# Kernel tuning notes

Hardware: AMD Instinct MI355X
Metric: run time of the kernel (lower is better)

The kernel has to match this reference:

```python
import jax, jax.numpy as jnp
import numpy as np

NUM_NODES = 50000
NUM_RELATIONS = 16
HIDDEN = 128
NUM_LAYERS = 3
NUM_EDGES = 1600000


def setup_inputs() -> dict:
    key = jax.random.key(0)
    ks = jax.random.split(key, 6)
    edge_index = jax.random.randint(ks[0], (2, NUM_EDGES), 0, NUM_NODES, dtype=jnp.int64)
    edge_type = jax.random.randint(ks[1], (NUM_EDGES,), 0, NUM_RELATIONS, dtype=jnp.int64)
    scale = 1.0 / np.sqrt(HIDDEN)
    node_init = jax.random.normal(ks[2], (NUM_NODES, HIDDEN), dtype=jnp.float32) * scale
    W = jax.random.normal(ks[3], (NUM_LAYERS, NUM_RELATIONS, HIDDEN, HIDDEN), dtype=jnp.float32) * scale
    root = jax.random.normal(ks[4], (NUM_LAYERS, HIDDEN, HIDDEN), dtype=jnp.float32) * scale
    bias = jnp.zeros((NUM_LAYERS, HIDDEN), dtype=jnp.float32)
    return {"edge_index": edge_index, "edge_type": edge_type,
            "node_init": node_init, "W": W, "root": root, "bias": bias}


def _fast_rgcn_layer(x, src, tgt, edge_type, W_r, root_r, bias_r):
    # FastRGCNConv with aggr='mean': mean of messages per (target node, relation),
    # message = x_src @ W[relation]. By linearity, aggregate normalized x_src per
    # (node, relation) first, then apply relation weights with a single einsum.
    N, d = x.shape
    R = W_r.shape[0]
    seg = tgt * R + edge_type                       # combined (node, relation) segment id
    msg = x[src]                                    # [E, d] irregular gather
    agg = jax.ops.segment_sum(msg, seg, num_segments=N * R).reshape(N, R, d)
    cnt = jax.ops.segment_sum(jnp.ones_like(edge_type, dtype=x.dtype), seg,
                              num_segments=N * R).reshape(N, R, 1)
    agg = agg / jnp.clip(cnt, 1.0, None)            # per-(node,relation) mean
    out = jnp.einsum('nrd,rdo->no', agg, W_r)       # relation-specific transform
    out = out + x @ root_r + bias_r                 # root/self connection + bias
    return out


def reference(edge_index, edge_type, node_init, W, root, bias):
    src, tgt = edge_index[0], edge_index[1]
    x = node_init
    for i in range(NUM_LAYERS):
        x = _fast_rgcn_layer(x, src, tgt, edge_type, W[i], root[i], bias[i])
        if i < NUM_LAYERS - 1:
            x = jax.nn.relu(x)  # dropout omitted (eval mode)
    return x
```

## Files before the change

### kernel.cpp

```cpp
#include <hip/hip_runtime.h>
#include <hip/hip_bf16.h>

#define N_NODES   50000
#define N_REL     16
#define HID       128
#define N_EDGES   1600000
#define N_TILES   3125
#define N_BINS    800000
#define N_RUNS    50000
#define N_SCANBLK 49
#define N_MBLK    1563
#define PAYLOAD_CAP 2400064
#define BS_LAYER  278528
#define AG_STRIDE 136

typedef unsigned short ushort_t;
typedef __attribute__((ext_vector_type(8))) short short8;
typedef __attribute__((ext_vector_type(4))) float f32x4;

union BF2U { __hip_bfloat162 h; unsigned u; };

__device__ __forceinline__ unsigned pack_bf16_2(float x, float y) {
  BF2U c; c.h = __float22bfloat162_rn(make_float2(x, y));
  return c.u;
}


__global__ __launch_bounds__(256) void k_zero(int* p, int n) {
  int i = blockIdx.x * 256 + threadIdx.x;
  if (i < n) p[i] = 0;
}

__global__ __launch_bounds__(256) void k_hist(const int* __restrict__ ei,
                                              const int* __restrict__ et,
                                              int* __restrict__ cnt) {
  int e = blockIdx.x * 256 + threadIdx.x;
  int tgt = ei[N_EDGES + e];
  int r   = et[e];
  int key = ((tgt >> 4) << 8) | (r << 4) | (tgt & 15);
  atomicAdd(&cnt[key], 1);
}

__global__ __launch_bounds__(256) void k_runpad(const int* __restrict__ cnt,
                                                int* __restrict__ padtot) {
  int r = blockIdx.x * 256 + threadIdx.x;
  if (r >= N_RUNS) return;
  const int4* c4 = (const int4*)(cnt + r * 16);
  int s = 0;
#pragma unroll
  for (int j = 0; j < 4; ++j) { int4 v = c4[j]; s += v.x + v.y + v.z + v.w; }
  padtot[r] = (s + 15) & ~15;
}

__global__ __launch_bounds__(256) void k_btot(const int* __restrict__ in,
                                              int* __restrict__ totals, int n) {
  __shared__ int s[256];
  int t = threadIdx.x, b = blockIdx.x;
  int sum = 0;
  for (int j = 0; j < 4; ++j) {
    int idx = b * 1024 + j * 256 + t;
    sum += (idx < n) ? in[idx] : 0;
  }
  s[t] = sum; __syncthreads();
  for (int ofs = 128; ofs > 0; ofs >>= 1) {
    if (t < ofs) s[t] += s[t + ofs];
    __syncthreads();
  }
  if (t == 0) totals[b] = s[0];
}

__global__ __launch_bounds__(1024) void k_scan_totals(int* totals, int* endp, int nblk) {
  __shared__ int s[1024];
  int t = threadIdx.x;
  int v = (t < nblk) ? totals[t] : 0;
  s[t] = v; __syncthreads();
  for (int ofs = 1; ofs < 1024; ofs <<= 1) {
    int x = (t >= ofs) ? s[t - ofs] : 0;
    __syncthreads();
    s[t] += x;
    __syncthreads();
  }
  if (t < nblk) totals[t] = s[t] - v;
  if (t == nblk - 1) *endp = s[t];
}

__global__ __launch_bounds__(1024) void k_scan_within(int* __restrict__ a,
                                                      const int* __restrict__ totals,
                                                      int n) {
  __shared__ int s[1024];
  int t = threadIdx.x, blk = blockIdx.x;
  int b = blk * 1024 + t;
  int v = (b < n) ? a[b] : 0;
  s[t] = v; __syncthreads();
  for (int ofs = 1; ofs < 1024; ofs <<= 1) {
    int x = (t >= ofs) ? s[t - ofs] : 0;
    __syncthreads();
    s[t] += x;
    __syncthreads();
  }
  if (b < n) a[b] = totals[blk] + s[t] - v;
}

__global__ __launch_bounds__(256) void k_fineoff(const int* __restrict__ cnt,
                                                 const int* __restrict__ run_start,
                                                 int* __restrict__ cursors,
                                                 unsigned* __restrict__ payload) {
  int r = blockIdx.x * 256 + threadIdx.x;
  if (r >= N_RUNS) return;
  int base = run_start[r];
  int e1   = run_start[r + 1];
  int pfx = 0;
  for (int i = 0; i < 16; ++i) {
    cursors[r * 16 + i] = base + pfx;
    pfx += cnt[r * 16 + i];
  }
  const unsigned dummy = ((unsigned)N_NODES << 16) | (1u << 4) | 15u;
  for (int j = base + pfx; j < e1; ++j) payload[j] = dummy;
}

__global__ __launch_bounds__(256) void k_sort(const int* __restrict__ ei,
                                              const int* __restrict__ et,
                                              const int* __restrict__ cnt,
                                              int* __restrict__ cursors,
                                              unsigned* __restrict__ payload) {
  int e = blockIdx.x * 256 + threadIdx.x;
  int src = ei[e];
  int tgt = ei[N_EDGES + e];
  int r   = et[e];
  int key = ((tgt >> 4) << 8) | (r << 4) | (tgt & 15);
  int c = cnt[key]; c = c > 4095 ? 4095 : c;
  int pos = atomicAdd(&cursors[key], 1);
  payload[pos] = ((unsigned)src << 16) | ((unsigned)c << 4) | (unsigned)(tgt & 15);
}

__global__ __launch_bounds__(256) void k_bt(const float* __restrict__ W,
                                            const float* __restrict__ root,
                                            ushort_t* __restrict__ Bs) {
  int idx = blockIdx.x * 256 + threadIdx.x;
  int l    = idx / BS_LAYER;
  int rem  = idx - l * BS_LAYER;
  int frag = rem >> 9;
  int wi   = rem & 511;
  int lane = wi >> 3;
  int j    = wi & 7;
  int cb   = frag & 7;
  int kk   = (frag >> 3) & 3;
  int r    = frag >> 5;
  int col  = cb * 16 + (lane & 15);
  int d    = kk * 32 + (lane >> 4) * 8 + j;
  float v;
  if (r < 16) v = W[((size_t)(l * N_REL + r) * HID + d) * HID + col];
  else        v = root[((size_t)l * HID + d) * HID + col];
  __hip_bfloat16 h = __float2bfloat16(v);
  union { __hip_bfloat16 h; ushort_t u; } c; c.h = h;
  Bs[idx] = c.u;
}

__global__ __launch_bounds__(256) void k_xh(const float* __restrict__ xin,
                                            ushort_t* __restrict__ xh) {
  int i = blockIdx.x * 256 + threadIdx.x;
  float4 v = ((const float4*)xin)[i];
  uint2 u;
  u.x = pack_bf16_2(v.x, v.y);
  u.y = pack_bf16_2(v.z, v.w);
  ((uint2*)xh)[i] = u;
}

__global__ __launch_bounds__(256) void k_zrow(ushort_t* xa, ushort_t* xb) {
  int t = threadIdx.x;
  if (t < 128) xa[(size_t)N_NODES * HID + t] = 0;
  else         xb[(size_t)N_NODES * HID + (t - 128)] = 0;
}


__global__ __launch_bounds__(256, 3) void k_main(const ushort_t* __restrict__ xh,
                                                 ushort_t* __restrict__ xh_out,
                                                 float* __restrict__ fout,
                                                 const ushort_t* __restrict__ Bs,
                                                 const float* __restrict__ bias,
                                                 const int* __restrict__ run_start,
                                                 const unsigned* __restrict__ payload,
                                                 int write_f32) {
  __shared__ alignas(16) ushort_t agg[2][2][32][AG_STRIDE];

  const int tile0 = blockIdx.x * 2;
  const int tid   = threadIdx.x;
  const int wave  = tid >> 6;
  const int lane  = tid & 63;
  const int m16   = lane & 15;
  const int q     = lane >> 4;
  const unsigned* xh32 = (const unsigned*)xh;

  if (wave < 2) {
    const int p = wave;
    int ebv = 0;
    {
      int s8 = lane >> 2, t2 = (lane >> 1) & 1, h = lane & 1;
      int tt = tile0 + t2;
      int idx = (tt < N_TILES) ? (tt * 16 + s8 * 2 + p + h) : N_RUNS;
      if (lane < 32) ebv = run_start[idx];
    }
    int pv[8][2];
#pragma unroll
    for (int s = 0; s < 8; ++s)
#pragma unroll
      for (int t = 0; t < 2; ++t) {
        int e0 = __builtin_amdgcn_readlane(ebv, s * 4 + t * 2);
        pv[s][t] = (int)payload[e0 + lane];
      }

#define ISSUE16(DST, PV, JB)                                                  \
    _Pragma("unroll")                                                         \
    for (int k1 = 0; k1 < 16; ++k1) {                                         \
      unsigned spq = (unsigned)__builtin_amdgcn_readlane(PV, (JB) + k1);      \
      DST[k1] = xh32[(spq >> 16) * 64 + lane];                                \
    }

#define FLUSHM(TB, BUF)                                                       \
    if (mcur >= 0) {                                                          \
      float sc = __builtin_amdgcn_rcpf((float)scnt);                          \
      *(unsigned*)&agg[BUF][p][(TB) + mcur][lane * 2] =                       \
          pack_bf16_2(a0 * sc, a1 * sc);                                      \
    }

#define CONSUME1(SPK, XV, TB, BUF)                                            \
    {                                                                         \
      int mk = (int)((SPK) & 15u);                                            \
      if (mk != mcur) {                                                       \
        FLUSHM(TB, BUF);                                                      \
        mcur = mk; scnt = (int)(((SPK) >> 4) & 4095u);                        \
        a0 = 0.f; a1 = 0.f;                                                   \
      }                                                                       \
      a0 += __uint_as_float((XV) << 16);                                      \
      a1 += __uint_as_float((XV) & 0xffff0000u);                              \
    }

#define CONS16(PV, JB, SLOT, TB, BUF)                                         \
    _Pragma("unroll")                                                         \
    for (int k2 = 0; k2 < 16; ++k2) {                                         \
      unsigned spk = (unsigned)__builtin_amdgcn_readlane(PV, (JB) + k2);      \
      CONSUME1(spk, SLOT[k2], TB, BUF);                                       \
    }

#define RUNC(E0, E1, PV, S0, S1a, S1b, TB, BUF)                               \
    {                                                                         \
      int cnt = (E1) - (E0);                                                  \
      int mcur = -1, scnt = 1;                                                \
      float a0 = 0.f, a1 = 0.f;                                               \
      if (cnt > 0) {                                                          \
        if (cnt > 16) { ISSUE16(S1a, PV, 16); }                               \
        CONS16(PV, 0, S0, TB, BUF);                                           \
        if (cnt > 16) {                                                       \
          if (cnt > 32) { ISSUE16(S1b, PV, 32); }                             \
          CONS16(PV, 16, S1a, TB, BUF);                                       \
          if (cnt > 32) {                                                     \
            if (cnt > 48) { ISSUE16(S1a, PV, 48); }                           \
            CONS16(PV, 32, S1b, TB, BUF);                                     \
            if (cnt > 48) { CONS16(PV, 48, S1a, TB, BUF); }                   \
          }                                                                   \
        }                                                                     \
        for (int c0 = (E0) + 64; c0 < (E1); c0 += 16) {             \
          int pvx = (int)payload[c0 + lane];                                  \
          unsigned xv[16];                                                    \
          ISSUE16(xv, pvx, 0);                                                \
          CONS16(pvx, 0, xv, TB, BUF);                                        \
        }                                                                     \
        FLUSHM(TB, BUF);                                                      \
      }                                                                       \
    }

    unsigned xqA[16], xqB[16], xqC[16], xqD[16];
    ISSUE16(xqA, pv[0][0], 0);
    ISSUE16(xqB, pv[0][1], 0);

#pragma unroll
    for (int s = 0; s < 8; ++s) {
      const int buf = s & 1;
      {
        short8 z = {0, 0, 0, 0, 0, 0, 0, 0};
#pragma unroll
        for (int i = 0; i < 8; ++i)
          *(short8*)&agg[buf][p][i * 4 + q][m16 * 8] = z;
      }
      int e00 = __builtin_amdgcn_readlane(ebv, s * 4 + 0);
      int e01 = __builtin_amdgcn_readlane(ebv, s * 4 + 1);
      int e10 = __builtin_amdgcn_readlane(ebv, s * 4 + 2);
      int e11 = __builtin_amdgcn_readlane(ebv, s * 4 + 3);
      RUNC(e00, e01, pv[s][0], xqA, xqC, xqD, 0, buf);
      RUNC(e10, e11, pv[s][1], xqB, xqC, xqD, 16, buf);
      if (s < 7) {
        ISSUE16(xqA, pv[s + 1][0], 0);
        ISSUE16(xqB, pv[s + 1][1], 0);
      }
      __syncthreads();
    }
#undef RUNC
#undef CONS16
#undef CONSUME1
#undef FLUSHM
#undef ISSUE16
    return;
  }

  const int c = wave - 2;
  f32x4 acc[2][4];
#pragma unroll
  for (int t = 0; t < 2; ++t)
#pragma unroll
    for (int i = 0; i < 4; ++i) acc[t][i] = (f32x4){0.f, 0.f, 0.f, 0.f};

  for (int s = 0; s < 8; ++s) {
    __syncthreads();
#pragma unroll
    for (int rp = 0; rp < 2; ++rp) {
      int rel = s * 2 + rp;
      short8 Bf[4][4];
#pragma unroll
      for (int kk = 0; kk < 4; ++kk)
#pragma unroll
        for (int i = 0; i < 4; ++i)
          Bf[kk][i] = *(const short8*)(Bs +
              ((size_t)((rel * 4 + kk) * 8 + (c * 4 + i)) << 9) + lane * 8);
#pragma unroll
      for (int kk = 0; kk < 4; ++kk) {
        short8 A0 = *(const short8*)&agg[s & 1][rp][m16][kk * 32 + q * 8];
        short8 A1 = *(const short8*)&agg[s & 1][rp][16 + m16][kk * 32 + q * 8];
#pragma unroll
        for (int i = 0; i < 4; ++i) {
          acc[0][i] = __builtin_amdgcn_mfma_f32_16x16x32_bf16(A0, Bf[kk][i], acc[0][i], 0, 0, 0);
          acc[1][i] = __builtin_amdgcn_mfma_f32_16x16x32_bf16(A1, Bf[kk][i], acc[1][i], 0, 0, 0);
        }
      }
    }
  }

  {
    short8 Bf[4][4];
#pragma unroll
    for (int kk = 0; kk < 4; ++kk)
#pragma unroll
      for (int i = 0; i < 4; ++i)
        Bf[kk][i] = *(const short8*)(Bs +
            ((size_t)((16 * 4 + kk) * 8 + (c * 4 + i)) << 9) + lane * 8);
    int r0 = tile0 * 16 + m16;      if (r0 > N_NODES) r0 = N_NODES;
    int r1 = tile0 * 16 + 16 + m16; if (r1 > N_NODES) r1 = N_NODES;
#pragma unroll
    for (int kk = 0; kk < 4; ++kk) {
      short8 A0 = *(const short8*)(xh + (size_t)r0 * HID + kk * 32 + q * 8);
      short8 A1 = *(const short8*)(xh + (size_t)r1 * HID + kk * 32 + q * 8);
#pragma unroll
      for (int i = 0; i < 4; ++i) {
        acc[0][i] = __builtin_amdgcn_mfma_f32_16x16x32_bf16(A0, Bf[kk][i], acc[0][i], 0, 0, 0);
        acc[1][i] = __builtin_amdgcn_mfma_f32_16x16x32_bf16(A1, Bf[kk][i], acc[1][i], 0, 0, 0);
      }
    }
  }

  float bvv[4];
#pragma unroll
  for (int i = 0; i < 4; ++i) bvv[i] = bias[(c * 4 + i) * 16 + m16];
  int rbase = tile0 * 16 + q * 4;
#pragma unroll
  for (int t = 0; t < 2; ++t)
#pragma unroll
    for (int rg = 0; rg < 4; ++rg) {
      int row = rbase + t * 16 + rg;
      if (row < N_NODES) {
#pragma unroll
        for (int i = 0; i < 4; ++i) {
          float v = acc[t][i][rg] + bvv[i];
          int col = (c * 4 + i) * 16 + m16;
          if (write_f32) {
            fout[(size_t)row * HID + col] = v;
          } else {
            v = fmaxf(v, 0.f);
            union { __hip_bfloat16 h; ushort_t u; } cv;
            cv.h = __float2bfloat16(v);
            xh_out[(size_t)row * HID + col] = cv.u;
          }
        }
      }
    }
}


extern "C" void kernel_launch(void* const* d_in, const int* in_sizes, int n_in,
                              void* d_out, int out_size, void* d_ws, size_t ws_size,
                              hipStream_t stream) {
  const int*   ei        = (const int*)d_in[0];
  const int*   et        = (const int*)d_in[1];
  const float* node_init = (const float*)d_in[2];
  const float* W         = (const float*)d_in[3];
  const float* root      = (const float*)d_in[4];
  const float* bias      = (const float*)d_in[5];
  float* outp = (float*)d_out;

  char* ws = (char*)d_ws;
  size_t o = 0;
  auto carve = [&](size_t bytes) { char* p = ws + o; o = (o + bytes + 255) & ~(size_t)255; return p; };
  ushort_t* xh_a      = (ushort_t*)carve((size_t)(N_NODES + 1) * HID * 2);
  ushort_t* xh_b      = (ushort_t*)carve((size_t)(N_NODES + 1) * HID * 2);
  unsigned* payload   = (unsigned*)carve((size_t)PAYLOAD_CAP * 4);
  int*      cnt       = (int*)     carve((size_t)N_BINS * 4);
  int*      cursors   = (int*)     carve((size_t)N_BINS * 4);
  int*      run_start = (int*)     carve((size_t)(N_RUNS + 1) * 4);
  int*      totals    = (int*)     carve((size_t)N_SCANBLK * 4);
  ushort_t* Bs        = (ushort_t*)carve((size_t)3 * BS_LAYER * 2);
  (void)ws_size; (void)n_in; (void)in_sizes; (void)out_size;

  hipLaunchKernelGGL(k_zero,        dim3(N_BINS / 256), dim3(256), 0, stream, cnt, N_BINS);
  hipLaunchKernelGGL(k_hist,        dim3(N_EDGES / 256), dim3(256), 0, stream, ei, et, cnt);
  hipLaunchKernelGGL(k_runpad,      dim3((N_RUNS + 255) / 256), dim3(256), 0, stream, cnt, run_start);
  hipLaunchKernelGGL(k_btot,        dim3(N_SCANBLK), dim3(256), 0, stream, run_start, totals, N_RUNS);
  hipLaunchKernelGGL(k_scan_totals, dim3(1), dim3(1024), 0, stream, totals, run_start + N_RUNS, N_SCANBLK);
  hipLaunchKernelGGL(k_scan_within, dim3(N_SCANBLK), dim3(1024), 0, stream, run_start, totals, N_RUNS);
  hipLaunchKernelGGL(k_fineoff,     dim3((N_RUNS + 255) / 256), dim3(256), 0, stream, cnt, run_start, cursors, payload);
  hipLaunchKernelGGL(k_sort,        dim3(N_EDGES / 256), dim3(256), 0, stream, ei, et, cnt, cursors, payload);
  hipLaunchKernelGGL(k_bt,          dim3(3 * BS_LAYER / 256), dim3(256), 0, stream, W, root, Bs);
  hipLaunchKernelGGL(k_xh,          dim3(N_NODES * HID / 4 / 256), dim3(256), 0, stream, node_init, xh_a);
  hipLaunchKernelGGL(k_zrow,        dim3(1), dim3(256), 0, stream, xh_a, xh_b);

  hipLaunchKernelGGL(k_main, dim3(N_MBLK), dim3(256), 0, stream,
                     xh_a, xh_b, (float*)nullptr,
                     Bs + (size_t)0 * BS_LAYER, bias + 0 * HID, run_start, payload, 0);
  hipLaunchKernelGGL(k_main, dim3(N_MBLK), dim3(256), 0, stream,
                     xh_b, xh_a, (float*)nullptr,
                     Bs + (size_t)1 * BS_LAYER, bias + 1 * HID, run_start, payload, 0);
  hipLaunchKernelGGL(k_main, dim3(N_MBLK), dim3(256), 0, stream,
                     xh_a, (ushort_t*)nullptr, outp,
                     Bs + (size_t)2 * BS_LAYER, bias + 2 * HID, run_start, payload, 1);
}
```

Before: 611.3 us.

## Reuse histogram ranks for sort, vectorize weight packing, and rework gather pipelining

```diff
diff --git a/kernel.cpp b/kernel.cpp
--- a/kernel.cpp
+++ b/kernel.cpp
@@ -25,20 +25,20 @@
   return c.u;
 }
 
-
-__global__ __launch_bounds__(256) void k_zero(int* p, int n) {
-  int i = blockIdx.x * 256 + threadIdx.x;
-  if (i < n) p[i] = 0;
-}
+__device__ __forceinline__ void lds_barrier() {
+  asm volatile("s_waitcnt lgkmcnt(0)\n\ts_barrier" ::: "memory");
+}
+
 
 __global__ __launch_bounds__(256) void k_hist(const int* __restrict__ ei,
                                               const int* __restrict__ et,
-                                              int* __restrict__ cnt) {
+                                              int* __restrict__ cnt,
+                                              int* __restrict__ rank) {
   int e = blockIdx.x * 256 + threadIdx.x;
   int tgt = ei[N_EDGES + e];
   int r   = et[e];
   int key = ((tgt >> 4) << 8) | (r << 4) | (tgt & 15);
-  atomicAdd(&cnt[key], 1);
+  rank[e] = atomicAdd(&cnt[key], 1);
 }
 
 __global__ __launch_bounds__(256) void k_runpad(const int* __restrict__ cnt,
@@ -103,7 +103,7 @@
 
 __global__ __launch_bounds__(256) void k_fineoff(const int* __restrict__ cnt,
                                                  const int* __restrict__ run_start,
-                                                 int* __restrict__ cursors,
+                                                 int* __restrict__ fine_start,
                                                  unsigned* __restrict__ payload) {
   int r = blockIdx.x * 256 + threadIdx.x;
   if (r >= N_RUNS) return;
@@ -111,7 +111,7 @@
   int e1   = run_start[r + 1];
   int pfx = 0;
   for (int i = 0; i < 16; ++i) {
-    cursors[r * 16 + i] = base + pfx;
+    fine_start[r * 16 + i] = base + pfx;
     pfx += cnt[r * 16 + i];
   }
   const unsigned dummy = ((unsigned)N_NODES << 16) | (1u << 4) | 15u;
@@ -121,7 +121,8 @@
 __global__ __launch_bounds__(256) void k_sort(const int* __restrict__ ei,
                                               const int* __restrict__ et,
                                               const int* __restrict__ cnt,
-                                              int* __restrict__ cursors,
+                                              const int* __restrict__ fine_start,
+                                              const int* __restrict__ rank,
                                               unsigned* __restrict__ payload) {
   int e = blockIdx.x * 256 + threadIdx.x;
   int src = ei[e];
@@ -129,7 +130,7 @@
   int r   = et[e];
   int key = ((tgt >> 4) << 8) | (r << 4) | (tgt & 15);
   int c = cnt[key]; c = c > 4095 ? 4095 : c;
-  int pos = atomicAdd(&cursors[key], 1);
+  int pos = fine_start[key] + rank[e];
   payload[pos] = ((unsigned)src << 16) | ((unsigned)c << 4) | (unsigned)(tgt & 15);
 }
 
@@ -137,23 +138,24 @@
                                             const float* __restrict__ root,
                                             ushort_t* __restrict__ Bs) {
   int idx = blockIdx.x * 256 + threadIdx.x;
-  int l    = idx / BS_LAYER;
-  int rem  = idx - l * BS_LAYER;
-  int frag = rem >> 9;
-  int wi   = rem & 511;
-  int lane = wi >> 3;
-  int j    = wi & 7;
-  int cb   = frag & 7;
-  int kk   = (frag >> 3) & 3;
-  int r    = frag >> 5;
-  int col  = cb * 16 + (lane & 15);
-  int d    = kk * 32 + (lane >> 4) * 8 + j;
-  float v;
-  if (r < 16) v = W[((size_t)(l * N_REL + r) * HID + d) * HID + col];
-  else        v = root[((size_t)l * HID + d) * HID + col];
-  __hip_bfloat16 h = __float2bfloat16(v);
-  union { __hip_bfloat16 h; ushort_t u; } c; c.h = h;
-  Bs[idx] = c.u;
+  int lane = idx & 63;
+  int fl   = idx >> 6;
+  int frag = fl % 544;
+  int l    = fl / 544;
+  int cb = frag & 7, kk = (frag >> 3) & 3, r = frag >> 5;
+  int col = cb * 16 + (lane & 15);
+  int d0  = kk * 32 + (lane >> 4) * 8;
+  const float* srcp = (r < 16)
+      ? W + ((size_t)(l * N_REL + r) * HID + d0) * HID + col
+      : root + ((size_t)l * HID + d0) * HID + col;
+  ushort_t out[8];
+#pragma unroll
+  for (int j = 0; j < 8; ++j) {
+    union { __hip_bfloat16 h; ushort_t u; } c;
+    c.h = __float2bfloat16(srcp[(size_t)j * HID]);
+    out[j] = c.u;
+  }
+  *(short8*)(Bs + ((size_t)fl << 9) + lane * 8) = *(short8*)out;
 }
 
 __global__ __launch_bounds__(256) void k_xh(const float* __restrict__ xin,
@@ -173,7 +175,7 @@
 }
 
 
-__global__ __launch_bounds__(256, 3) void k_main(const ushort_t* __restrict__ xh,
+__global__ __launch_bounds__(256, 4) void k_main(const ushort_t* __restrict__ xh,
                                                  ushort_t* __restrict__ xh_out,
                                                  float* __restrict__ fout,
                                                  const ushort_t* __restrict__ Bs,
@@ -200,14 +202,6 @@
       int idx = (tt < N_TILES) ? (tt * 16 + s8 * 2 + p + h) : N_RUNS;
       if (lane < 32) ebv = run_start[idx];
     }
-    int pv[8][2];
-#pragma unroll
-    for (int s = 0; s < 8; ++s)
-#pragma unroll
-      for (int t = 0; t < 2; ++t) {
-        int e0 = __builtin_amdgcn_readlane(ebv, s * 4 + t * 2);
-        pv[s][t] = (int)payload[e0 + lane];
-      }
 
 #define ISSUE16(DST, PV, JB)                                                  \
     _Pragma("unroll")                                                         \
@@ -242,59 +236,81 @@
       CONSUME1(spk, SLOT[k2], TB, BUF);                                       \
     }
 
-#define RUNC(E0, E1, PV, S0, S1a, S1b, TB, BUF)                               \
+#define RUNX(PV, E0, E1, CNT, B0, B1, TB)                                     \
     {                                                                         \
-      int cnt = (E1) - (E0);                                                  \
       int mcur = -1, scnt = 1;                                                \
       float a0 = 0.f, a1 = 0.f;                                               \
-      if (cnt > 0) {                                                          \
-        if (cnt > 16) { ISSUE16(S1a, PV, 16); }                               \
-        CONS16(PV, 0, S0, TB, BUF);                                           \
-        if (cnt > 16) {                                                       \
-          if (cnt > 32) { ISSUE16(S1b, PV, 32); }                             \
-          CONS16(PV, 16, S1a, TB, BUF);                                       \
-          if (cnt > 32) {                                                     \
-            if (cnt > 48) { ISSUE16(S1a, PV, 48); }                           \
-            CONS16(PV, 32, S1b, TB, BUF);                                     \
-            if (cnt > 48) { CONS16(PV, 48, S1a, TB, BUF); }                   \
+      if ((CNT) > 0) {                                                        \
+        CONS16(PV, 0, B0, TB, buf);                                           \
+        if ((CNT) > 16) {                                                     \
+          CONS16(PV, 16, B1, TB, buf);                                        \
+          if ((CNT) > 32) {                                                   \
+            CONS16(PV, 32, xqE, TB, buf);                                     \
+            if ((CNT) > 48) {                                                 \
+              ISSUE16(xqE, PV, 48);                                           \
+              CONS16(PV, 48, xqE, TB, buf);                                   \
+            }                                                                 \
           }                                                                   \
         }                                                                     \
-        for (int c0 = (E0) + 64; c0 < (E1); c0 += 16) {             \
+        for (int c0 = (E0) + 64; c0 < (E1); c0 += 16) {        \
           int pvx = (int)payload[c0 + lane];                                  \
-          unsigned xv[16];                                                    \
-          ISSUE16(xv, pvx, 0);                                                \
-          CONS16(pvx, 0, xv, TB, BUF);                                        \
+          ISSUE16(xqE, pvx, 0);                                               \
+          CONS16(pvx, 0, xqE, TB, buf);                                       \
         }                                                                     \
-        FLUSHM(TB, BUF);                                                      \
+        FLUSHM(TB, buf);                                                      \
       }                                                                       \
     }
 
-    unsigned xqA[16], xqB[16], xqC[16], xqD[16];
-    ISSUE16(xqA, pv[0][0], 0);
-    ISSUE16(xqB, pv[0][1], 0);
-
-#pragma unroll
+    unsigned xqA[16], xqB[16], xqC[16], xqD[16], xqE[16];
+
+    int e00 = __builtin_amdgcn_readlane(ebv, 0);
+    int e01 = __builtin_amdgcn_readlane(ebv, 1);
+    int e10 = __builtin_amdgcn_readlane(ebv, 2);
+    int e11 = __builtin_amdgcn_readlane(ebv, 3);
+    int pv0 = (int)payload[e00 + lane];
+    int pv1 = (int)payload[e10 + lane];
+    ISSUE16(xqA, pv0, 0);
+    ISSUE16(xqC, pv1, 0);
+
     for (int s = 0; s < 8; ++s) {
       const int buf = s & 1;
+      int cnt0 = e01 - e00, cnt1 = e11 - e10;
+
+      if (cnt0 > 16) ISSUE16(xqB, pv0, 16);
+      if (cnt1 > 16) ISSUE16(xqD, pv1, 16);
+      if (cnt0 > 32) ISSUE16(xqE, pv0, 32);
+
+      int f00 = e00, f01 = e01, f10 = e10, f11 = e11;
+      int pvn0 = pv0, pvn1 = pv1;
+      if (s < 7) {
+        f00 = __builtin_amdgcn_readlane(ebv, (s + 1) * 4 + 0);
+        f01 = __builtin_amdgcn_readlane(ebv, (s + 1) * 4 + 1);
+        f10 = __builtin_amdgcn_readlane(ebv, (s + 1) * 4 + 2);
+        f11 = __builtin_amdgcn_readlane(ebv, (s + 1) * 4 + 3);
+        pvn0 = (int)payload[f00 + lane];
+        pvn1 = (int)payload[f10 + lane];
+      }
+
       {
         short8 z = {0, 0, 0, 0, 0, 0, 0, 0};
 #pragma unroll
         for (int i = 0; i < 8; ++i)
           *(short8*)&agg[buf][p][i * 4 + q][m16 * 8] = z;
       }
-      int e00 = __builtin_amdgcn_readlane(ebv, s * 4 + 0);
-      int e01 = __builtin_amdgcn_readlane(ebv, s * 4 + 1);
-      int e10 = __builtin_amdgcn_readlane(ebv, s * 4 + 2);
-      int e11 = __builtin_amdgcn_readlane(ebv, s * 4 + 3);
-      RUNC(e00, e01, pv[s][0], xqA, xqC, xqD, 0, buf);
-      RUNC(e10, e11, pv[s][1], xqB, xqC, xqD, 16, buf);
+
+      RUNX(pv0, e00, e01, cnt0, xqA, xqB, 0);
+      if (cnt1 > 32) ISSUE16(xqE, pv1, 32);
+      RUNX(pv1, e10, e11, cnt1, xqC, xqD, 16);
+
       if (s < 7) {
-        ISSUE16(xqA, pv[s + 1][0], 0);
-        ISSUE16(xqB, pv[s + 1][1], 0);
-      }
-      __syncthreads();
-    }
-#undef RUNC
+        e00 = f00; e01 = f01; e10 = f10; e11 = f11;
+        pv0 = pvn0; pv1 = pvn1;
+        ISSUE16(xqA, pv0, 0);
+        ISSUE16(xqC, pv1, 0);
+      }
+      lds_barrier();
+    }
+#undef RUNX
 #undef CONS16
 #undef CONSUME1
 #undef FLUSHM
@@ -310,7 +326,7 @@
     for (int i = 0; i < 4; ++i) acc[t][i] = (f32x4){0.f, 0.f, 0.f, 0.f};
 
   for (int s = 0; s < 8; ++s) {
-    __syncthreads();
+    lds_barrier();
 #pragma unroll
     for (int rp = 0; rp < 2; ++rp) {
       int rel = s * 2 + rp;
@@ -398,25 +414,26 @@
   char* ws = (char*)d_ws;
   size_t o = 0;
   auto carve = [&](size_t bytes) { char* p = ws + o; o = (o + bytes + 255) & ~(size_t)255; return p; };
-  ushort_t* xh_a      = (ushort_t*)carve((size_t)(N_NODES + 1) * HID * 2);
-  ushort_t* xh_b      = (ushort_t*)carve((size_t)(N_NODES + 1) * HID * 2);
-  unsigned* payload   = (unsigned*)carve((size_t)PAYLOAD_CAP * 4);
-  int*      cnt       = (int*)     carve((size_t)N_BINS * 4);
-  int*      cursors   = (int*)     carve((size_t)N_BINS * 4);
-  int*      run_start = (int*)     carve((size_t)(N_RUNS + 1) * 4);
-  int*      totals    = (int*)     carve((size_t)N_SCANBLK * 4);
-  ushort_t* Bs        = (ushort_t*)carve((size_t)3 * BS_LAYER * 2);
+  ushort_t* xh_a       = (ushort_t*)carve((size_t)(N_NODES + 1) * HID * 2);
+  ushort_t* xh_b       = (ushort_t*)carve((size_t)(N_NODES + 1) * HID * 2);
+  unsigned* payload    = (unsigned*)carve((size_t)PAYLOAD_CAP * 4);
+  int*      cnt        = (int*)     carve((size_t)N_BINS * 4);
+  int*      fine_start = (int*)     carve((size_t)N_BINS * 4);
+  int*      rank       = (int*)     carve((size_t)N_EDGES * 4);
+  int*      run_start  = (int*)     carve((size_t)(N_RUNS + 1) * 4);
+  int*      totals     = (int*)     carve((size_t)N_SCANBLK * 4);
+  ushort_t* Bs         = (ushort_t*)carve((size_t)3 * BS_LAYER * 2);
   (void)ws_size; (void)n_in; (void)in_sizes; (void)out_size;
 
-  hipLaunchKernelGGL(k_zero,        dim3(N_BINS / 256), dim3(256), 0, stream, cnt, N_BINS);
-  hipLaunchKernelGGL(k_hist,        dim3(N_EDGES / 256), dim3(256), 0, stream, ei, et, cnt);
+  hipMemsetAsync(cnt, 0, (size_t)N_BINS * 4, stream);
+  hipLaunchKernelGGL(k_hist,        dim3(N_EDGES / 256), dim3(256), 0, stream, ei, et, cnt, rank);
   hipLaunchKernelGGL(k_runpad,      dim3((N_RUNS + 255) / 256), dim3(256), 0, stream, cnt, run_start);
   hipLaunchKernelGGL(k_btot,        dim3(N_SCANBLK), dim3(256), 0, stream, run_start, totals, N_RUNS);
   hipLaunchKernelGGL(k_scan_totals, dim3(1), dim3(1024), 0, stream, totals, run_start + N_RUNS, N_SCANBLK);
   hipLaunchKernelGGL(k_scan_within, dim3(N_SCANBLK), dim3(1024), 0, stream, run_start, totals, N_RUNS);
-  hipLaunchKernelGGL(k_fineoff,     dim3((N_RUNS + 255) / 256), dim3(256), 0, stream, cnt, run_start, cursors, payload);
-  hipLaunchKernelGGL(k_sort,        dim3(N_EDGES / 256), dim3(256), 0, stream, ei, et, cnt, cursors, payload);
-  hipLaunchKernelGGL(k_bt,          dim3(3 * BS_LAYER / 256), dim3(256), 0, stream, W, root, Bs);
+  hipLaunchKernelGGL(k_fineoff,     dim3((N_RUNS + 255) / 256), dim3(256), 0, stream, cnt, run_start, fine_start, payload);
+  hipLaunchKernelGGL(k_sort,        dim3(N_EDGES / 256), dim3(256), 0, stream, ei, et, cnt, fine_start, rank, payload);
+  hipLaunchKernelGGL(k_bt,          dim3(3 * 544 * 64 / 256), dim3(256), 0, stream, W, root, Bs);
   hipLaunchKernelGGL(k_xh,          dim3(N_NODES * HID / 4 / 256), dim3(256), 0, stream, node_init, xh_a);
   hipLaunchKernelGGL(k_zrow,        dim3(1), dim3(256), 0, stream, xh_a, xh_b);
 
```

Result: no change. 611.7 us (+0.1%).
